# Optimization experiments

Hardware: AMD Instinct MI355X
Metric: run time of the kernel (lower is better)

## Reference

```python
import jax, jax.numpy as jnp
import numpy as np

B, S, D, H = 4, 2048, 1024, 16
HD = D // H

def setup_inputs() -> dict:
    key = jax.random.key(0)
    ks = jax.random.split(key, 12)
    std = 1.0 / np.sqrt(D)
    inp = {
        'query': jax.random.normal(ks[0], (B, S, D), jnp.float32),
        'key':   jax.random.normal(ks[1], (B, S, D), jnp.float32),
        'value': jax.random.normal(ks[2], (B, S, D), jnp.float32),
        'mask':  jnp.tril(jnp.ones((S, S), jnp.int32))[None, None, :, :],  # [1,1,S,S] causal
        'Wq': jax.random.uniform(ks[3], (D, D), jnp.float32, -std, std),
        'bq': jax.random.uniform(ks[4], (D,), jnp.float32, -std, std),
        'Wk': jax.random.uniform(ks[5], (D, D), jnp.float32, -std, std),
        'bk': jax.random.uniform(ks[6], (D,), jnp.float32, -std, std),
        'Wv': jax.random.uniform(ks[7], (D, D), jnp.float32, -std, std),
        'bv': jax.random.uniform(ks[8], (D,), jnp.float32, -std, std),
        'Wo': jax.random.uniform(ks[9], (D, D), jnp.float32, -std, std),
        'bo': jax.random.uniform(ks[10], (D,), jnp.float32, -std, std),
    }
    return inp

def _split_heads(x, W, b):
    # torch Linear: x @ W.T + b ; then [B,S,H,HD] -> [B,H,S,HD]
    y = jnp.einsum('bsd,ed->bse', x, W) + b
    return y.reshape(x.shape[0], -1, H, HD).transpose(0, 2, 1, 3)

def reference(query, key, value, mask, Wq, bq, Wk, bk, Wv, bv, Wo, bo):
    q = _split_heads(query, Wq, bq)   # [B,H,S,HD]
    k = _split_heads(key,   Wk, bk)
    v = _split_heads(value, Wv, bv)
    logits = jnp.einsum('bhqd,bhkd->bhqk', q, k) / np.sqrt(HD)  # [B,H,S,S]
    logits = jnp.where(mask == 0, jnp.float32(-1e9), logits)
    attn = jax.nn.softmax(logits, axis=-1)
    out = jnp.einsum('bhqk,bhkd->bhqd', attn, v)               # [B,H,S,HD]
    out = out.transpose(0, 2, 1, 3).reshape(query.shape[0], -1, D)
    return jnp.einsum('bsd,ed->bse', out, Wo) + bo
```

## Files before the change

### kernel.cpp

```cpp
#include <hip/hip_runtime.h>
#include <hip/hip_bf16.h>


#define SLEN 2048
#define DMOD 1024

typedef __attribute__((ext_vector_type(8))) short s16x8;
typedef __attribute__((ext_vector_type(4))) float f32x4;

__device__ __forceinline__ unsigned short f2bf(float f) {
    union { __hip_bfloat16 h; unsigned short u; } cv;
    cv.h = __float2bfloat16(f);
    return cv.u;
}
__device__ __forceinline__ unsigned cvtpk(float a, float b) {
    unsigned r;
    asm("v_cvt_pk_bf16_f32 %0, %1, %2" : "=v"(r) : "v"(a), "v"(b));
    return r;
}

__device__ __forceinline__ void gload_lds16(const void* g, void* l) {
    __builtin_amdgcn_global_load_lds(
        (const __attribute__((address_space(1))) void*)g,
        (__attribute__((address_space(3))) void*)l, 16, 0, 0);
}

__global__ __launch_bounds__(256) void convert_bf16(
    const float* __restrict__ q, const float* __restrict__ k,
    const float* __restrict__ v, const float* __restrict__ wq,
    const float* __restrict__ wk, const float* __restrict__ wv,
    const float* __restrict__ wo, unsigned short* __restrict__ ws)
{
    const int bid = blockIdx.x, tid = threadIdx.x;
    const float* src;
    unsigned short* dst;
    size_t off;
    if (bid < 3072) {
        const int t = bid >> 10;
        src = (t == 0) ? q : (t == 1) ? k : v;
        dst = ws + (size_t)t * 8388608;
        off = (size_t)(bid & 1023) * 8192;
    } else {
        const int w = (bid - 3072) >> 7;
        src = (w == 0) ? wq : (w == 1) ? wk : (w == 2) ? wv : wo;
        dst = ws + 25165824 + (size_t)w * 1048576;
        off = (size_t)((bid - 3072) & 127) * 8192;
    }
#pragma unroll
    for (int i = 0; i < 8; ++i) {
        const size_t e = off + (size_t)(i * 256 + tid) * 4;
        float4 x = *reinterpret_cast<const float4*>(&src[e]);
        uint2 u;
        u.x = cvtpk(x.x, x.y);
        u.y = cvtpk(x.z, x.w);
        *reinterpret_cast<uint2*>(&dst[e]) = u;
    }
}

template<int MODE>
__global__ __launch_bounds__(256) void gemm_bf16(
    const unsigned short* __restrict__ A, const unsigned short* __restrict__ W,
    const float* __restrict__ bias, void* __restrict__ outp)
{
    __shared__ unsigned short Asm[2][8192];
    __shared__ unsigned short Bsm[2][8192];

    const int tid  = threadIdx.x;
    const int lane = tid & 63, wid = tid >> 6;
    const int l15 = lane & 15, lhi = lane >> 4;

    const int flat = blockIdx.x;
    const int logical = (flat & 7) * 64 + (flat >> 3);
    const int m0 = (logical >> 3) * 128, n0 = (logical & 7) * 128;

    const int wr = wid >> 1, wc = wid & 1;
    const int srow = lane >> 3;
    const int sgr  = (lane & 7) ^ srow;

    int aoff[2][4], boff[2][4];
#pragma unroll
    for (int kk = 0; kk < 2; ++kk)
#pragma unroll
        for (int i = 0; i < 4; ++i) {
            const int s = ((4 * kk + lhi) ^ (l15 & 7)) * 16;
            aoff[kk][i] = (wr * 64 + i * 16 + l15) * 128 + s;
            boff[kk][i] = (wc * 64 + i * 16 + l15) * 128 + s;
        }

    const unsigned short* apt = A + (size_t)(m0 + wid * 8 + srow) * 1024 + sgr * 8;
    const unsigned short* bpt = W + (size_t)(n0 + wid * 8 + srow) * 1024 + sgr * 8;

    f32x4 acc[4][4];
#pragma unroll
    for (int i = 0; i < 4; ++i)
#pragma unroll
        for (int j = 0; j < 4; ++j) acc[i][j] = (f32x4)0.f;

    auto stage = [&](int bsel) {
        char* ad = (char*)Asm + bsel * 16384 + wid * 1024;
        char* bd = (char*)Bsm + bsel * 16384 + wid * 1024;
#pragma unroll
        for (int i = 0; i < 4; ++i) {
            gload_lds16(apt + i * 32768, ad + i * 4096);
            gload_lds16(bpt + i * 32768, bd + i * 4096);
        }
        apt += 64; bpt += 64;
    };

    stage(0);
    __syncthreads();
    int cur = 0;
#pragma unroll 1
    for (int kt = 0; kt < 16; ++kt) {
        if (kt < 15) stage(cur ^ 1);
        const char* AB = (const char*)Asm + cur * 16384;
        const char* BB = (const char*)Bsm + cur * 16384;
#pragma unroll
        for (int kk = 0; kk < 2; ++kk) {
            s16x8 af[4], bfv[4];
#pragma unroll
            for (int i = 0; i < 4; ++i) af[i]  = *reinterpret_cast<const s16x8*>(AB + aoff[kk][i]);
#pragma unroll
            for (int j = 0; j < 4; ++j) bfv[j] = *reinterpret_cast<const s16x8*>(BB + boff[kk][j]);
#pragma unroll
            for (int i = 0; i < 4; ++i)
#pragma unroll
                for (int j = 0; j < 4; ++j)
                    acc[i][j] = __builtin_amdgcn_mfma_f32_16x16x32_bf16(af[i], bfv[j], acc[i][j], 0, 0, 0);
        }
        __syncthreads();
        cur ^= 1;
    }

#pragma unroll
    for (int j = 0; j < 4; ++j) {
        const int col = n0 + wc * 64 + j * 16 + l15;
        const float bv = bias[col];
#pragma unroll
        for (int i = 0; i < 4; ++i) {
#pragma unroll
            for (int r = 0; r < 4; ++r) {
                const int row = m0 + wr * 64 + i * 16 + lhi * 4 + r;
                const float val = acc[i][j][r] + bv;
                if constexpr (MODE == 2) {
                    ((float*)outp)[(size_t)row * 1024 + col] = val;
                } else if constexpr (MODE == 0) {
                    ((unsigned short*)outp)[(size_t)((row >> 11) * 16 + (col >> 6)) * 131072
                                            + (size_t)(row & 2047) * 64 + (col & 63)] = f2bf(val);
                } else {
                    ((unsigned short*)outp)[(size_t)((row >> 11) * 16 + (col >> 6)) * 131072
                                            + (size_t)(col & 63) * 2048 + (row & 2047)] = f2bf(val);
                }
            }
        }
    }
}

#define EXPC 0.18033688011112043f

__global__ __launch_bounds__(256, 4) void attn_kernel(
    const unsigned short* __restrict__ Q,
    const unsigned short* __restrict__ Kc,
    const unsigned short* __restrict__ Vt,
    unsigned short* __restrict__ Ao)
{
    __shared__ unsigned short Kbuf[2][4096];
    __shared__ unsigned short Vbuf[2][4096];
    __shared__ unsigned short Psm[4][1024];

    const int tid = threadIdx.x, lane = tid & 63, wid = tid >> 6;
    const int l15 = lane & 15, lhi = lane >> 4;
    const int sK = l15 & 7;
    const int sub = lane >> 3, c8s = lane & 7;
    const int thr = wid * 16 + l15;

    int ko[8], pr[2], pw[4];
#pragma unroll
    for (int kk = 0; kk < 2; ++kk) {
        pr[kk] = (l15 * 8 + ((4 * kk + lhi) ^ sK)) * 16;
#pragma unroll
        for (int nb = 0; nb < 4; ++nb)
            ko[kk * 4 + nb] = ((nb * 16 + l15) * 8 + ((4 * kk + lhi) ^ sK)) * 16;
    }
#pragma unroll
    for (int nb = 0; nb < 4; ++nb)
        pw[nb] = (l15 * 16 + ((nb * 4 + lhi) ^ (2 * sK))) * 8;

    const int flat = blockIdx.x;
    const int logical = (flat & 7) * 128 + (flat >> 3);
    const int bx = logical & 15, bh = logical >> 4;

    const size_t base = (size_t)bh * SLEN * 64;
    const unsigned short* Qb = Q + base;
    const unsigned short* Kb = Kc + base;
    const unsigned short* Vb = Vt + base;
    const int b = bh >> 4, h = bh & 15;
    const int scol = (c8s ^ sub) * 8;

    const f32x4 fzero = (f32x4)0.f;
    const s16x8 onesb = (s16x8)(short)0x3F80;

#pragma unroll 1
    for (int seg = 0; seg < 2; ++seg) {
        const int qt = seg ? (31 - bx) : bx;
        const int q0 = qt * 64;

        s16x8 aq[2];
#pragma unroll
        for (int kk = 0; kk < 2; ++kk)
            aq[kk] = *reinterpret_cast<const s16x8*>(
                &Qb[(size_t)(q0 + wid * 16 + l15) * 64 + kk * 32 + 8 * lhi]);

        f32x4 o_acc[4];
#pragma unroll
        for (int nb = 0; nb < 4; ++nb) o_acc[nb] = (f32x4)0.f;
        f32x4 l_acc = (f32x4)0.f;
        float m_r = -1e30f;

        const unsigned short* kpt = Kb + (16 * wid + sub) * 64 + scol;
        const unsigned short* vpt = Vb + (size_t)(16 * wid + sub) * SLEN + scol;

        auto stage = [&](int bsel) {
            char* kd = (char*)Kbuf + bsel * 8192 + wid * 2048;
            char* vd = (char*)Vbuf + bsel * 8192 + wid * 2048;
            gload_lds16(kpt,         kd);
            gload_lds16(kpt + 512,   kd + 1024);
            gload_lds16(vpt,         vd);
            gload_lds16(vpt + 16384, vd + 1024);
            kpt += 4096; vpt += 64;
        };

        auto tile = [&](int cbo, bool domask) {
            const char* KB = (const char*)Kbuf + cbo;
            const char* VB = (const char*)Vbuf + cbo;
            char* PW = (char*)Psm + wid * 2048;

            f32x4 sc2[4];
            __builtin_amdgcn_s_setprio(1);
#pragma unroll
            for (int kk = 0; kk < 2; ++kk) {
                s16x8 ak[4];
#pragma unroll
                for (int nb = 0; nb < 4; ++nb)
                    ak[nb] = *reinterpret_cast<const s16x8*>(KB + ko[kk * 4 + nb]);
#pragma unroll
                for (int nb = 0; nb < 4; ++nb)
                    sc2[nb] = __builtin_amdgcn_mfma_f32_16x16x32_bf16(
                        ak[nb], aq[kk], kk == 0 ? fzero : sc2[nb], 0, 0, 0);
            }
            __builtin_amdgcn_s_setprio(0);

            if (domask) {
#pragma unroll
                for (int nb = 0; nb < 4; ++nb)
#pragma unroll
                    for (int r = 0; r < 4; ++r)
                        if (nb * 16 + lhi * 4 + r > thr) sc2[nb][r] = -3e30f;
            }
            float tm[4];
#pragma unroll
            for (int nb = 0; nb < 4; ++nb)
                tm[nb] = fmaxf(fmaxf(sc2[nb][0], sc2[nb][1]),
                               fmaxf(sc2[nb][2], sc2[nb][3]));
            float tmx = fmaxf(fmaxf(tm[0], tm[1]), fmaxf(tm[2], tm[3]));

            if (__any(tmx - m_r > 64.0f)) {
                float tf = fmaxf(tmx, __shfl_xor(tmx, 16));
                tf = fmaxf(tf, __shfl_xor(tf, 32));
                const float mn = fmaxf(m_r, tf);
                const float alpha = exp2f((m_r - mn) * EXPC);
                m_r = mn;
                float ar[4];
#pragma unroll
                for (int r = 0; r < 4; ++r) ar[r] = __shfl(alpha, lhi * 4 + r);
#pragma unroll
                for (int r = 0; r < 4; ++r) l_acc[r] *= ar[r];
#pragma unroll
                for (int nb = 0; nb < 4; ++nb)
#pragma unroll
                    for (int r = 0; r < 4; ++r) o_acc[nb][r] *= ar[r];
            }

            const float negmC = -m_r * EXPC;
#pragma unroll
            for (int nb = 0; nb < 4; ++nb) {
                float p0 = exp2f(fmaf(sc2[nb][0], EXPC, negmC));
                float p1 = exp2f(fmaf(sc2[nb][1], EXPC, negmC));
                float p2 = exp2f(fmaf(sc2[nb][2], EXPC, negmC));
                float p3 = exp2f(fmaf(sc2[nb][3], EXPC, negmC));
                uint2 u;
                u.x = cvtpk(p0, p1);
                u.y = cvtpk(p2, p3);
                *reinterpret_cast<uint2*>(PW + pw[nb]) = u;
            }

            __builtin_amdgcn_s_setprio(1);
#pragma unroll
            for (int kk = 0; kk < 2; ++kk) {
                s16x8 pa = *reinterpret_cast<const s16x8*>(PW + pr[kk]);
                s16x8 bvv[4];
#pragma unroll
                for (int nb = 0; nb < 4; ++nb)
                    bvv[nb] = *reinterpret_cast<const s16x8*>(VB + ko[kk * 4 + nb]);
#pragma unroll
                for (int nb = 0; nb < 4; ++nb)
                    o_acc[nb] = __builtin_amdgcn_mfma_f32_16x16x32_bf16(pa, bvv[nb], o_acc[nb], 0, 0, 0);
                l_acc = __builtin_amdgcn_mfma_f32_16x16x32_bf16(pa, onesb, l_acc, 0, 0, 0);
            }
            __builtin_amdgcn_s_setprio(0);
        };

        stage(0);
        __syncthreads();
        int cur = 0;

#pragma unroll 1
        for (int t = 0; t < qt; ++t) {
            stage(cur ^ 1);
            tile(cur * 8192, false);
            __syncthreads();
            cur ^= 1;
        }
        tile(cur * 8192, true);

        float linv[4];
#pragma unroll
        for (int r = 0; r < 4; ++r) linv[r] = 1.0f / l_acc[r];
#pragma unroll
        for (int nb = 0; nb < 4; ++nb)
#pragma unroll
            for (int r = 0; r < 4; ++r) {
                const int s = q0 + wid * 16 + lhi * 4 + r;
                Ao[((size_t)b * SLEN + s) * DMOD + h * 64 + nb * 16 + l15] =
                    f2bf(o_acc[nb][r] * linv[r]);
            }
        __syncthreads();
    }
}

extern "C" void kernel_launch(void* const* d_in, const int* in_sizes, int n_in,
                              void* d_out, int out_size, void* d_ws, size_t ws_size,
                              hipStream_t stream) {
    const float* q  = (const float*)d_in[0];
    const float* k  = (const float*)d_in[1];
    const float* v  = (const float*)d_in[2];
    const float* Wq = (const float*)d_in[4];
    const float* bq = (const float*)d_in[5];
    const float* Wk = (const float*)d_in[6];
    const float* bk = (const float*)d_in[7];
    const float* Wv = (const float*)d_in[8];
    const float* bv = (const float*)d_in[9];
    const float* Wo = (const float*)d_in[10];
    const float* bo = (const float*)d_in[11];

    unsigned short* wsp = (unsigned short*)d_ws;
    unsigned short* qc  = wsp;
    unsigned short* kc  = wsp + 8388608;
    unsigned short* vc  = wsp + 16777216;
    unsigned short* wqc = wsp + 25165824;
    unsigned short* wkc = wsp + 26214400;
    unsigned short* wvc = wsp + 27262976;
    unsigned short* woc = wsp + 28311552;
    unsigned short* qb  = wsp + 29360128;
    unsigned short* kb  = wsp + 37748736;
    unsigned short* vtb = wsp + 46137344;
    unsigned short* ao  = qc;

    dim3 gb(256);
    convert_bf16<<<dim3(3584), gb, 0, stream>>>(q, k, v, Wq, Wk, Wv, Wo, wsp);
    gemm_bf16<0><<<dim3(512), gb, 0, stream>>>(qc, wqc, bq, qb);
    gemm_bf16<0><<<dim3(512), gb, 0, stream>>>(kc, wkc, bk, kb);
    gemm_bf16<1><<<dim3(512), gb, 0, stream>>>(vc, wvc, bv, vtb);
    attn_kernel<<<dim3(1024), gb, 0, stream>>>(qb, kb, vtb, ao);
    gemm_bf16<2><<<dim3(512), gb, 0, stream>>>(ao, woc, bo, (float*)d_out);
}
```

Before: 188.0 us.

## Fuse fp32-to-bf16 conversion into GEMM staging via register prefetch

Drops the separate conversion kernel and has each projection GEMM read fp32 activations and weights directly, converting them to bf16 in registers before storing to shared memory. The async global-to-LDS loads are replaced by register prefetch of the next tile, which overlaps with the MFMA work on the current tile. This removes a full write and re-read of bf16 copies of the inputs and one kernel launch. In exchange the GEMM fetches twice the bytes per tile (fp32 weights, which each block re-reads), uses more registers for staging, and now requests two blocks per CU through launch bounds.

```diff
diff --git a/kernel.cpp b/kernel.cpp
--- a/kernel.cpp
+++ b/kernel.cpp
@@ -25,41 +25,9 @@
         (__attribute__((address_space(3))) void*)l, 16, 0, 0);
 }
 
-__global__ __launch_bounds__(256) void convert_bf16(
-    const float* __restrict__ q, const float* __restrict__ k,
-    const float* __restrict__ v, const float* __restrict__ wq,
-    const float* __restrict__ wk, const float* __restrict__ wv,
-    const float* __restrict__ wo, unsigned short* __restrict__ ws)
-{
-    const int bid = blockIdx.x, tid = threadIdx.x;
-    const float* src;
-    unsigned short* dst;
-    size_t off;
-    if (bid < 3072) {
-        const int t = bid >> 10;
-        src = (t == 0) ? q : (t == 1) ? k : v;
-        dst = ws + (size_t)t * 8388608;
-        off = (size_t)(bid & 1023) * 8192;
-    } else {
-        const int w = (bid - 3072) >> 7;
-        src = (w == 0) ? wq : (w == 1) ? wk : (w == 2) ? wv : wo;
-        dst = ws + 25165824 + (size_t)w * 1048576;
-        off = (size_t)((bid - 3072) & 127) * 8192;
-    }
-#pragma unroll
-    for (int i = 0; i < 8; ++i) {
-        const size_t e = off + (size_t)(i * 256 + tid) * 4;
-        float4 x = *reinterpret_cast<const float4*>(&src[e]);
-        uint2 u;
-        u.x = cvtpk(x.x, x.y);
-        u.y = cvtpk(x.z, x.w);
-        *reinterpret_cast<uint2*>(&dst[e]) = u;
-    }
-}
-
-template<int MODE>
-__global__ __launch_bounds__(256) void gemm_bf16(
-    const unsigned short* __restrict__ A, const unsigned short* __restrict__ W,
+template<int MODE, bool ABF>
+__global__ __launch_bounds__(256, 2) void gemm_v4(
+    const void* __restrict__ Aptr, const float* __restrict__ Wp,
     const float* __restrict__ bias, void* __restrict__ outp)
 {
     __shared__ unsigned short Asm[2][8192];
@@ -72,10 +40,16 @@
     const int flat = blockIdx.x;
     const int logical = (flat & 7) * 64 + (flat >> 3);
     const int m0 = (logical >> 3) * 128, n0 = (logical & 7) * 128;
-
     const int wr = wid >> 1, wc = wid & 1;
-    const int srow = lane >> 3;
-    const int sgr  = (lane & 7) ^ srow;
+
+    int srow[4], sg[4], soff[4];
+#pragma unroll
+    for (int i = 0; i < 4; ++i) {
+        const int f = i * 256 + tid;
+        srow[i] = f >> 3;
+        sg[i]   = f & 7;
+        soff[i] = srow[i] * 128 + ((sg[i] ^ (srow[i] & 7)) * 16);
+    }
 
     int aoff[2][4], boff[2][4];
 #pragma unroll
@@ -87,34 +61,70 @@
             boff[kk][i] = (wc * 64 + i * 16 + l15) * 128 + s;
         }
 
-    const unsigned short* apt = A + (size_t)(m0 + wid * 8 + srow) * 1024 + sgr * 8;
-    const unsigned short* bpt = W + (size_t)(n0 + wid * 8 + srow) * 1024 + sgr * 8;
-
     f32x4 acc[4][4];
 #pragma unroll
     for (int i = 0; i < 4; ++i)
 #pragma unroll
         for (int j = 0; j < 4; ++j) acc[i][j] = (f32x4)0.f;
 
-    auto stage = [&](int bsel) {
-        char* ad = (char*)Asm + bsel * 16384 + wid * 1024;
-        char* bd = (char*)Bsm + bsel * 16384 + wid * 1024;
+    float4 aw[8], ww[8];
+    int4 ab[4];
+
+    auto loadS = [&](int k0) {
+        if constexpr (ABF) {
+            const unsigned short* Af = (const unsigned short*)Aptr;
+#pragma unroll
+            for (int i = 0; i < 4; ++i)
+                ab[i] = *reinterpret_cast<const int4*>(
+                    &Af[(size_t)(m0 + srow[i]) * 1024 + k0 + sg[i] * 8]);
+        } else {
+            const float* Af = (const float*)Aptr;
+#pragma unroll
+            for (int i = 0; i < 4; ++i) {
+                const float* s = &Af[(size_t)(m0 + srow[i]) * 1024 + k0 + sg[i] * 8];
+                aw[2 * i]     = *reinterpret_cast<const float4*>(s);
+                aw[2 * i + 1] = *reinterpret_cast<const float4*>(s + 4);
+            }
+        }
 #pragma unroll
         for (int i = 0; i < 4; ++i) {
-            gload_lds16(apt + i * 32768, ad + i * 4096);
-            gload_lds16(bpt + i * 32768, bd + i * 4096);
-        }
-        apt += 64; bpt += 64;
+            const float* s = &Wp[(size_t)(n0 + srow[i]) * 1024 + k0 + sg[i] * 8];
+            ww[2 * i]     = *reinterpret_cast<const float4*>(s);
+            ww[2 * i + 1] = *reinterpret_cast<const float4*>(s + 4);
+        }
     };
 
-    stage(0);
+    auto writeS = [&](int bsel) {
+#pragma unroll
+        for (int i = 0; i < 4; ++i) {
+            if constexpr (ABF) {
+                *reinterpret_cast<int4*>((char*)&Asm[bsel][0] + soff[i]) = ab[i];
+            } else {
+                uint4 u;
+                u.x = cvtpk(aw[2 * i].x,     aw[2 * i].y);
+                u.y = cvtpk(aw[2 * i].z,     aw[2 * i].w);
+                u.z = cvtpk(aw[2 * i + 1].x, aw[2 * i + 1].y);
+                u.w = cvtpk(aw[2 * i + 1].z, aw[2 * i + 1].w);
+                *reinterpret_cast<uint4*>((char*)&Asm[bsel][0] + soff[i]) = u;
+            }
+            uint4 w;
+            w.x = cvtpk(ww[2 * i].x,     ww[2 * i].y);
+            w.y = cvtpk(ww[2 * i].z,     ww[2 * i].w);
+            w.z = cvtpk(ww[2 * i + 1].x, ww[2 * i + 1].y);
+            w.w = cvtpk(ww[2 * i + 1].z, ww[2 * i + 1].w);
+            *reinterpret_cast<uint4*>((char*)&Bsm[bsel][0] + soff[i]) = w;
+        }
+    };
+
+    loadS(0);
+    writeS(0);
     __syncthreads();
-    int cur = 0;
+
 #pragma unroll 1
     for (int kt = 0; kt < 16; ++kt) {
-        if (kt < 15) stage(cur ^ 1);
-        const char* AB = (const char*)Asm + cur * 16384;
-        const char* BB = (const char*)Bsm + cur * 16384;
+        if (kt < 15) loadS((kt + 1) * 64);
+        const char* AB = (const char*)&Asm[kt & 1][0];
+        const char* BB = (const char*)&Bsm[kt & 1][0];
 #pragma unroll
         for (int kk = 0; kk < 2; ++kk) {
             s16x8 af[4], bfv[4];
@@ -128,8 +138,8 @@
                 for (int j = 0; j < 4; ++j)
                     acc[i][j] = __builtin_amdgcn_mfma_f32_16x16x32_bf16(af[i], bfv[j], acc[i][j], 0, 0, 0);
         }
+        if (kt < 15) writeS((kt + 1) & 1);
         __syncthreads();
-        cur ^= 1;
     }
 
 #pragma unroll
@@ -354,23 +364,15 @@
     const float* bo = (const float*)d_in[11];
 
     unsigned short* wsp = (unsigned short*)d_ws;
-    unsigned short* qc  = wsp;
-    unsigned short* kc  = wsp + 8388608;
-    unsigned short* vc  = wsp + 16777216;
-    unsigned short* wqc = wsp + 25165824;
-    unsigned short* wkc = wsp + 26214400;
-    unsigned short* wvc = wsp + 27262976;
-    unsigned short* woc = wsp + 28311552;
-    unsigned short* qb  = wsp + 29360128;
-    unsigned short* kb  = wsp + 37748736;
-    unsigned short* vtb = wsp + 46137344;
-    unsigned short* ao  = qc;
+    unsigned short* qb  = wsp;
+    unsigned short* kb  = wsp + 8388608;
+    unsigned short* vtb = wsp + 16777216;
+    unsigned short* ao  = wsp + 25165824;
 
     dim3 gb(256);
-    convert_bf16<<<dim3(3584), gb, 0, stream>>>(q, k, v, Wq, Wk, Wv, Wo, wsp);
-    gemm_bf16<0><<<dim3(512), gb, 0, stream>>>(qc, wqc, bq, qb);
-    gemm_bf16<0><<<dim3(512), gb, 0, stream>>>(kc, wkc, bk, kb);
-    gemm_bf16<1><<<dim3(512), gb, 0, stream>>>(vc, wvc, bv, vtb);
+    gemm_v4<0, false><<<dim3(512), gb, 0, stream>>>(q, Wq, bq, qb);
+    gemm_v4<0, false><<<dim3(512), gb, 0, stream>>>(k, Wk, bk, kb);
+    gemm_v4<1, false><<<dim3(512), gb, 0, stream>>>(v, Wv, bv, vtb);
     attn_kernel<<<dim3(1024), gb, 0, stream>>>(qb, kb, vtb, ao);
-    gemm_bf16<2><<<dim3(512), gb, 0, stream>>>(ao, woc, bo, (float*)d_out);
-}
+    gemm_v4<2, true><<<dim3(512), gb, 0, stream>>>(ao, Wo, bo, (float*)d_out);
+}
```

Measured after the change: 212.8 us. 1.13x slower.
